# Performance work log

Measured on AMD Instinct MI355X. Metric: run time of the kernel, lower is better.

## Reference

```python
import jax, jax.numpy as jnp
import numpy as np

B, T, EMBED_DIM = 8, 4096, 1024
NUM_HEADS = 16
D_K = EMBED_DIM // NUM_HEADS  # 64, equals n_wires


def setup_inputs() -> dict:
    key = jax.random.key(0)
    k1, k2 = jax.random.split(key)
    x = jax.random.normal(k1, (B, T, EMBED_DIM), dtype=jnp.float32)
    circuit_params = jax.random.normal(k2, (NUM_HEADS, D_K), dtype=jnp.float32)
    return {"x": x, "circuit_params": circuit_params}


def reference(x, circuit_params):
    # Closed form of the per-head circuit: RX(x_w)|0>, RZ(p_w) (diagonal ->
    # no effect on Z expectations), CNOT chain, <Z_k>.
    # Heisenberg: Z_k -> Z_0 Z_1 ... Z_k through the CNOT chain; product state
    # gives <Z_k> = prod_{w<=k} cos(x_w). circuit_params drop out analytically.
    Bs, Ts, C = x.shape
    xh = x.reshape(Bs, Ts, NUM_HEADS, D_K)  # wire axis last, same layout as torch view
    out = jnp.cumprod(jnp.cos(xh), axis=-1)
    return out.reshape(Bs, Ts, C)
```

## Files before the change

### kernel.cpp

```cpp
#include <hip/hip_runtime.h>


typedef float f32x4 __attribute__((ext_vector_type(4)));

__global__ __launch_bounds__(256) void quantum_cumprod_cos_kernel(
    const f32x4* __restrict__ x, f32x4* __restrict__ out, int nchunks) {
    const int tid    = blockIdx.x * blockDim.x + threadIdx.x;
    const int stride = gridDim.x * blockDim.x;

    for (int i = tid; i < nchunks; i += stride) {
        const int sub = i & 15;

        const f32x4 v = x[i];
        const float c0 = __cosf(v.x);
        const float c1 = __cosf(v.y);
        const float c2 = __cosf(v.z);
        const float c3 = __cosf(v.w);
        const float p0 = c0;
        const float p1 = p0 * c1;
        const float p2 = p1 * c2;
        const float p3 = p2 * c3;

        float e = __shfl_up(p3, 1, 16);
        if (sub == 0) e = 1.0f;
#pragma unroll
        for (int d = 1; d < 16; d <<= 1) {
            const float t = __shfl_up(e, d, 16);
            if (sub >= d) e *= t;
        }

        f32x4 o;
        o.x = e * p0;
        o.y = e * p1;
        o.z = e * p2;
        o.w = e * p3;
        __builtin_nontemporal_store(o, &out[i]);
    }
}

extern "C" void kernel_launch(void* const* d_in, const int* in_sizes, int n_in,
                              void* d_out, int out_size, void* d_ws, size_t ws_size,
                              hipStream_t stream) {
    (void)d_ws; (void)ws_size; (void)n_in;
    const f32x4* x = (const f32x4*)d_in[0];
    f32x4* out = (f32x4*)d_out;

    const int nchunks = out_size / 4;
    const int threads = 256;
    int blocks = (nchunks + threads - 1) / threads;
    if (blocks > 2048) blocks = 2048;

    quantum_cumprod_cos_kernel<<<blocks, threads, 0, stream>>>(x, out, nchunks);
}
```

Before: 45.75 us.

## Process sixteen elements per thread and shrink the shuffle scan to four lanes

Each thread now loads four consecutive float4 chunks (16 elements) and computes their running cosine product serially. The cross-thread scan drops from a 16-lane to a 4-lane shuffle. The grid-stride loop is replaced by one pass per thread with an uncapped grid. Per-thread loads now have a 64-byte stride across lanes instead of contiguous 16-byte accesses, which may hurt coalescing, and the serial multiply chain is longer.

Result: slower. 88.25 us (+92.9%).

```diff
diff --git a/kernel.cpp b/kernel.cpp
--- a/kernel.cpp
+++ b/kernel.cpp
@@ -4,38 +4,52 @@
 typedef float f32x4 __attribute__((ext_vector_type(4)));
 
 __global__ __launch_bounds__(256) void quantum_cumprod_cos_kernel(
-    const f32x4* __restrict__ x, f32x4* __restrict__ out, int nchunks) {
-    const int tid    = blockIdx.x * blockDim.x + threadIdx.x;
-    const int stride = gridDim.x * blockDim.x;
+    const f32x4* __restrict__ x, f32x4* __restrict__ out, int nthreads) {
+    const int t = blockIdx.x * blockDim.x + threadIdx.x;
+    if (t >= nthreads) return;
+    const int sub = t & 3;
 
-    for (int i = tid; i < nchunks; i += stride) {
-        const int sub = i & 15;
+    f32x4 v0 = x[t * 4 + 0];
+    f32x4 v1 = x[t * 4 + 1];
+    f32x4 v2 = x[t * 4 + 2];
+    f32x4 v3 = x[t * 4 + 3];
 
-        const f32x4 v = x[i];
-        const float c0 = __cosf(v.x);
-        const float c1 = __cosf(v.y);
-        const float c2 = __cosf(v.z);
-        const float c3 = __cosf(v.w);
-        const float p0 = c0;
-        const float p1 = p0 * c1;
-        const float p2 = p1 * c2;
-        const float p3 = p2 * c3;
+    float p[16];
+    p[0] = __cosf(v0.x);
+    p[1] = p[0] * __cosf(v0.y);
+    p[2] = p[1] * __cosf(v0.z);
+    p[3] = p[2] * __cosf(v0.w);
+    p[4] = p[3] * __cosf(v1.x);
+    p[5] = p[4] * __cosf(v1.y);
+    p[6] = p[5] * __cosf(v1.z);
+    p[7] = p[6] * __cosf(v1.w);
+    p[8] = p[7] * __cosf(v2.x);
+    p[9] = p[8] * __cosf(v2.y);
+    p[10] = p[9] * __cosf(v2.z);
+    p[11] = p[10] * __cosf(v2.w);
+    p[12] = p[11] * __cosf(v3.x);
+    p[13] = p[12] * __cosf(v3.y);
+    p[14] = p[13] * __cosf(v3.z);
+    p[15] = p[14] * __cosf(v3.w);
 
-        float e = __shfl_up(p3, 1, 16);
-        if (sub == 0) e = 1.0f;
-#pragma unroll
-        for (int d = 1; d < 16; d <<= 1) {
-            const float t = __shfl_up(e, d, 16);
-            if (sub >= d) e *= t;
-        }
+    const float pl = p[15];
+    float e = __shfl_up(pl, 1, 4);
+    if (sub == 0) e = 1.0f;
+    {
+        const float t1 = __shfl_up(e, 1, 4);
+        if (sub >= 1) e *= t1;
+        const float t2 = __shfl_up(e, 2, 4);
+        if (sub >= 2) e *= t2;
+    }
 
-        f32x4 o;
-        o.x = e * p0;
-        o.y = e * p1;
-        o.z = e * p2;
-        o.w = e * p3;
-        __builtin_nontemporal_store(o, &out[i]);
-    }
+    f32x4 o0 = {e * p[0], e * p[1], e * p[2], e * p[3]};
+    f32x4 o1 = {e * p[4], e * p[5], e * p[6], e * p[7]};
+    f32x4 o2 = {e * p[8], e * p[9], e * p[10], e * p[11]};
+    f32x4 o3 = {e * p[12], e * p[13], e * p[14], e * p[15]};
+    __builtin_nontemporal_store(o0, &out[t * 4 + 0]);
+    __builtin_nontemporal_store(o1, &out[t * 4 + 1]);
+    __builtin_nontemporal_store(o2, &out[t * 4 + 2]);
+    __builtin_nontemporal_store(o3, &out[t * 4 + 3]);
 }
 
 extern "C" void kernel_launch(void* const* d_in, const int* in_sizes, int n_in,
@@ -45,10 +59,9 @@
     const f32x4* x = (const f32x4*)d_in[0];
     f32x4* out = (f32x4*)d_out;
 
-    const int nchunks = out_size / 4;
+    const int nthreads = out_size / 16;
     const int threads = 256;
-    int blocks = (nchunks + threads - 1) / threads;
-    if (blocks > 2048) blocks = 2048;
+    const int blocks = (nthreads + threads - 1) / threads;
 
-    quantum_cumprod_cos_kernel<<<blocks, threads, 0, stream>>>(x, out, nchunks);
+    quantum_cumprod_cos_kernel<<<blocks, threads, 0, stream>>>(x, out, nthreads);
 }
```
